# Performance work log

Measured on AMD Instinct MI355X. Metric: run time of the kernel, lower is better.

## Reference

```python
import jax, jax.numpy as jnp
import numpy as np

D_MODEL = 1024
NUM_HEADS = 16
SEQ_LEN = 2048
WINDOW_SIZES = (5, 10, 20, 40)


def _avg_gaussian_mask(seq_len, dtype=jnp.float32):
    # mask[i,j] = exp(-(i-j)^2/(2 w^2)) if j <= i else 0; averaged over 4 windows.
    i = jnp.arange(seq_len, dtype=dtype)[:, None]
    j = jnp.arange(seq_len, dtype=dtype)[None, :]
    d2 = (i - j) ** 2
    lower = (j <= i)
    masks = [jnp.where(lower, jnp.exp(-d2 / (2.0 * w * w)), 0.0) for w in WINDOW_SIZES]
    return sum(masks) / len(WINDOW_SIZES)  # [S, S]


def setup_inputs() -> dict:
    key = jax.random.key(0)
    ks = jax.random.split(key, 11)
    B, S, D = 2, SEQ_LEN, D_MODEL
    std = 1.0 / np.sqrt(D)
    inp = {
        "Q": jax.random.normal(ks[0], (B, S, D), jnp.float32),
        "K": jax.random.normal(ks[1], (B, S, D), jnp.float32),
        "V": jax.random.normal(ks[2], (B, S, D), jnp.float32),
        "Wq": jax.random.uniform(ks[3], (D, D), jnp.float32, -std, std),
        "bq": jax.random.uniform(ks[4], (D,), jnp.float32, -std, std),
        "Wk": jax.random.uniform(ks[5], (D, D), jnp.float32, -std, std),
        "bk": jax.random.uniform(ks[6], (D,), jnp.float32, -std, std),
        "Wv": jax.random.uniform(ks[7], (D, D), jnp.float32, -std, std),
        "bv": jax.random.uniform(ks[8], (D,), jnp.float32, -std, std),
        "Wo": jax.random.uniform(ks[9], (D, D), jnp.float32, -std, std),
        "bo": jax.random.uniform(ks[10], (D,), jnp.float32, -std, std),
    }
    return inp


def reference(Q, K, V, Wq, bq, Wk, bk, Wv, bv, Wo, bo):
    B, S, D = Q.shape
    H, dk = NUM_HEADS, D // NUM_HEADS

    def proj(x, W, b):
        # torch Linear: x @ W^T + b, then split heads -> [B, H, S, dk]
        y = x @ W.T + b
        return y.reshape(B, S, H, dk).transpose(0, 2, 1, 3)

    q = proj(Q, Wq, bq)
    k = proj(K, Wk, bk)
    v = proj(V, Wv, bv)

    # mean over mask dim of (scores + mask_m) == scores + mean(mask)
    avg_mask = _avg_gaussian_mask(S, q.dtype)  # [S, S]
    scores = jnp.einsum('bhqd,bhkd->bhqk', q, k) / jnp.sqrt(jnp.asarray(dk, q.dtype))
    scores = scores + avg_mask  # broadcast over [B, H]
    probs = jax.nn.softmax(scores, axis=-1)
    out = jnp.einsum('bhqk,bhkd->bhqd', probs, v)
    out = out.transpose(0, 2, 1, 3).reshape(B, S, D)
    return out @ Wo.T + bo
```

## Files before the change

kernel.cpp:

```cpp
#include <hip/hip_runtime.h>
#include <hip/hip_bf16.h>


#define S_LEN 2048
#define D_MODEL 1024
#define NHEADS 16
#define DK 64
#define BATCH 2
#define M_ROWS (BATCH * S_LEN)
#define LOG2E 1.4426950408889634f

typedef float f32x4 __attribute__((ext_vector_type(4)));
typedef short s16x8 __attribute__((ext_vector_type(8)));
typedef unsigned short u16x4 __attribute__((ext_vector_type(4)));
typedef unsigned u32x2 __attribute__((ext_vector_type(2)));

__device__ __forceinline__ unsigned short f2bf(float f) {
    unsigned u = __builtin_bit_cast(unsigned, f);
    u = (u + 0x7FFFu + ((u >> 16) & 1u)) >> 16;
    return (unsigned short)u;
}

__device__ __forceinline__ float fast_exp2(float x) {
    float r;
    asm("v_exp_f32 %0, %1" : "=v"(r) : "v"(x));
    return r;
}

__device__ __forceinline__ unsigned cvt_pk_bf16(float a, float b) {
    unsigned r;
    asm("v_cvt_pk_bf16_f32 %0, %1, %2" : "=v"(r) : "v"(a), "v"(b));
    return r;
}

__device__ __forceinline__ float max3f(float a, float b, float c) {
    float r;
    asm("v_max3_f32 %0, %1, %2, %3" : "=v"(r) : "v"(a), "v"(b), "v"(c));
    return r;
}

#define GLD16(gptr, lptr)                                                     \
    __builtin_amdgcn_global_load_lds(                                         \
        (const __attribute__((address_space(1))) void*)(gptr),                \
        (__attribute__((address_space(3))) void*)(lptr), 16, 0, 0)

__global__ void mask_kernel(float* __restrict__ mtab) {
    int d = blockIdx.x * 256 + threadIdx.x;
    if (d < S_LEN) {
        float d2 = (float)d * (float)d;
        mtab[d] = LOG2E * 0.25f * (__expf(-d2 * (1.0f / 50.0f)) +
                                   __expf(-d2 * (1.0f / 200.0f)) +
                                   __expf(-d2 * (1.0f / 800.0f)) +
                                   __expf(-d2 * (1.0f / 3200.0f)));
    }
}

__global__ __launch_bounds__(256) void convert_kernel(
    const float* __restrict__ Q, const float* __restrict__ K,
    const float* __restrict__ V,
    const float* __restrict__ Wq, const float* __restrict__ Wk,
    const float* __restrict__ Wv, const float* __restrict__ Wo,
    unsigned short* __restrict__ Qb, unsigned short* __restrict__ Kb,
    unsigned short* __restrict__ Vb,
    unsigned short* __restrict__ Wqb, unsigned short* __restrict__ Wkb,
    unsigned short* __restrict__ Wvb, unsigned short* __restrict__ Wob)
{
    const int XN = M_ROWS * D_MODEL / 8;
    const int WN = D_MODEL * D_MODEL / 8;
    int i = blockIdx.x * 256 + threadIdx.x;
    const float* src;
    unsigned short* dst;
    int off;
    if (i < 3 * XN) {
        if (i < XN)          { src = Q; dst = Qb; off = i; }
        else if (i < 2 * XN) { src = K; dst = Kb; off = i - XN; }
        else                 { src = V; dst = Vb; off = i - 2 * XN; }
    } else {
        int j = i - 3 * XN;
        if (j < WN)          { src = Wq; dst = Wqb; off = j; }
        else if (j < 2 * WN) { src = Wk; dst = Wkb; off = j - WN; }
        else if (j < 3 * WN) { src = Wv; dst = Wvb; off = j - 2 * WN; }
        else                 { src = Wo; dst = Wob; off = j - 3 * WN; }
    }
    f32x4 v0 = *(const f32x4*)(src + (size_t)off * 8);
    f32x4 v1 = *(const f32x4*)(src + (size_t)off * 8 + 4);
    s16x8 o;
#pragma unroll
    for (int j = 0; j < 4; ++j) {
        o[j]     = (short)f2bf(v0[j]);
        o[j + 4] = (short)f2bf(v1[j]);
    }
    *(s16x8*)(dst + (size_t)off * 8) = o;
}

__device__ __forceinline__ void gemm_core_128(
    const unsigned short* __restrict__ A, const unsigned short* __restrict__ B,
    unsigned short* As, unsigned short* Bs,
    int m0, int n0, int K, int tid, f32x4 acc[4][4])
{
    const int wid  = tid >> 6;
    const int lane = tid & 63;
    const int g    = lane >> 4;
    const int c    = lane & 15;
    const int wm   = wid >> 1;
    const int wn   = wid & 1;

    const int srow   = tid >> 3;
    const int schunk = tid & 7;

    for (int kt = 0; kt < K / 64; ++kt) {
        const int k0 = kt * 64;
        __syncthreads();
#pragma unroll
        for (int r = 0; r < 4; ++r) {
            const int row = r * 32 + srow;
            GLD16(A + (size_t)(m0 + row) * K + k0 + schunk * 8,
                  &As[(r * 256 + wid * 64) * 8]);
        }
#pragma unroll
        for (int r = 0; r < 4; ++r) {
            const int row = r * 32 + srow;
            GLD16(B + (size_t)(n0 + row) * K + k0 + schunk * 8,
                  &Bs[(r * 256 + wid * 64) * 8]);
        }
        __syncthreads();

        s16x8 a[2][4];
#pragma unroll
        for (int ks = 0; ks < 2; ++ks)
#pragma unroll
            for (int mf = 0; mf < 4; ++mf)
                a[ks][mf] = *(const s16x8*)
                    &As[(wm * 64 + mf * 16 + c) * 64 + ks * 32 + g * 8];
#pragma unroll
        for (int ks = 0; ks < 2; ++ks) {
#pragma unroll
            for (int nf = 0; nf < 4; ++nf) {
                s16x8 b = *(const s16x8*)
                    &Bs[(wn * 64 + nf * 16 + c) * 64 + ks * 32 + g * 8];
#pragma unroll
                for (int mf = 0; mf < 4; ++mf)
                    acc[mf][nf] = __builtin_amdgcn_mfma_f32_16x16x32_bf16(
                        a[ks][mf], b, acc[mf][nf], 0, 0, 0);
            }
        }
    }
}

__global__ __launch_bounds__(256) void proj_gemm(
    const unsigned short* __restrict__ Qx, const unsigned short* __restrict__ Kx,
    const unsigned short* __restrict__ Vx,
    const unsigned short* __restrict__ Wq, const unsigned short* __restrict__ Wk,
    const unsigned short* __restrict__ Wv,
    const float* __restrict__ bq, const float* __restrict__ bk,
    const float* __restrict__ bv,
    unsigned short* __restrict__ qo, unsigned short* __restrict__ ko,
    unsigned short* __restrict__ vo)
{
    const int z = blockIdx.z;
    const unsigned short* X = (z == 0) ? Qx : (z == 1) ? Kx : Vx;
    const unsigned short* W = (z == 0) ? Wq : (z == 1) ? Wk : Wv;
    const float* bias       = (z == 0) ? bq : (z == 1) ? bk : bv;
    unsigned short* out     = (z == 0) ? qo : (z == 1) ? ko : vo;
    const float scale = (z == 0) ? (0.125f * LOG2E) : 1.0f;

    __shared__ unsigned short As[128 * 64];
    __shared__ unsigned short Bs[128 * 64];

    const int tid = threadIdx.x;
    const int m0  = blockIdx.x * 128;
    const int n0  = blockIdx.y * 128;

    f32x4 acc[4][4];
#pragma unroll
    for (int i = 0; i < 4; ++i)
#pragma unroll
        for (int j = 0; j < 4; ++j) acc[i][j] = (f32x4){0.f, 0.f, 0.f, 0.f};

    gemm_core_128(X, W, As, Bs, m0, n0, D_MODEL, tid, acc);

    const int lane = tid & 63;
    const int g    = lane >> 4;
    const int c    = lane & 15;
    const int wm   = (tid >> 6) >> 1;
    const int wn   = (tid >> 6) & 1;

#pragma unroll
    for (int mf = 0; mf < 4; ++mf) {
#pragma unroll
        for (int nf = 0; nf < 4; ++nf) {
            const int o = n0 + wn * 64 + nf * 16 + c;
            const float bv_ = bias[o];
            const int h  = o >> 6;
            const int dd = o & 63;
#pragma unroll
            for (int r = 0; r < 4; ++r) {
                const int m = m0 + wm * 64 + mf * 16 + g * 4 + r;
                const int b = m >> 11;
                const int s = m & (S_LEN - 1);
                const float val = (acc[mf][nf][r] + bv_) * scale;
                out[(((size_t)(b * NHEADS + h)) * S_LEN + s) * DK + dd] = f2bf(val);
            }
        }
    }
}

__global__ __launch_bounds__(256) void out_gemm(
    const unsigned short* __restrict__ A,
    const unsigned short* __restrict__ W,
    const float* __restrict__ bias,
    float* __restrict__ out)
{
    __shared__ unsigned short As[128 * 64];
    __shared__ unsigned short Bs[128 * 64];

    const int tid = threadIdx.x;
    const int m0  = blockIdx.x * 128;
    const int n0  = blockIdx.y * 128;

    f32x4 acc[4][4];
#pragma unroll
    for (int i = 0; i < 4; ++i)
#pragma unroll
        for (int j = 0; j < 4; ++j) acc[i][j] = (f32x4){0.f, 0.f, 0.f, 0.f};

    gemm_core_128(A, W, As, Bs, m0, n0, D_MODEL, tid, acc);

    const int lane = tid & 63;
    const int g    = lane >> 4;
    const int c    = lane & 15;
    const int wm   = (tid >> 6) >> 1;
    const int wn   = (tid >> 6) & 1;

#pragma unroll
    for (int mf = 0; mf < 4; ++mf) {
#pragma unroll
        for (int nf = 0; nf < 4; ++nf) {
            const int o = n0 + wn * 64 + nf * 16 + c;
            const float bv_ = bias[o];
#pragma unroll
            for (int r = 0; r < 4; ++r) {
                const int m = m0 + wm * 64 + mf * 16 + g * 4 + r;
                out[(size_t)m * D_MODEL + o] = acc[mf][nf][r] + bv_;
            }
        }
    }
}

#define VSWZ(row) ((((row) >> 1) & 7) << 4)

__global__ __launch_bounds__(512) void attn_kernel(
    const unsigned short* __restrict__ qh,
    const unsigned short* __restrict__ kh,
    const unsigned short* __restrict__ vh,
    const float* __restrict__ mask_tab,
    unsigned short* __restrict__ attn_out)
{
    __shared__ float mtab[S_LEN];
    __shared__ unsigned short Kt[64 * 64];
    __shared__ unsigned short Vt[64 * 64];
    __shared__ unsigned short Pt[8][16 * 64];

    const int tid  = threadIdx.x;
    const int wid  = tid >> 6;
    const int lane = tid & 63;
    const int g    = lane >> 4;
    const int c    = lane & 15;
    const int bh   = blockIdx.y;
    const int b    = bh >> 4;
    const int h    = bh & 15;
    const int q0w  = blockIdx.x * 128 + wid * 16;

    *(f32x4*)&mtab[tid * 4] = *(const f32x4*)&mask_tab[tid * 4];

    const size_t head_off = (size_t)bh * S_LEN * DK;
    const unsigned short* qp = qh + head_off;
    const unsigned short* kp = kh + head_off;
    const unsigned short* vp = vh + head_off;

    s16x8 aq[2];
    {
        const unsigned short* qrow = qp + (size_t)(q0w + c) * DK;
        aq[0] = *(const s16x8*)(qrow + g * 8);
        aq[1] = *(const s16x8*)(qrow + 32 + g * 8);
    }

    f32x4 acc_o[4];
#pragma unroll
    for (int nf = 0; nf < 4; ++nf) acc_o[nf] = (f32x4){0.f, 0.f, 0.f, 0.f};
    float m_l = -1e30f, l_l = 0.f;

    const int srowK = tid >> 3;
    const int soffE = (tid & 7) * 8;
    const int vd0   = (tid & 31) * 2;
    const int vkq   = (tid >> 5) * 4;

    s16x8 kreg;
    unsigned vreg[4];
    kreg = *(const s16x8*)&kp[(size_t)srowK * DK + soffE];
#pragma unroll
    for (int i = 0; i < 4; ++i)
        vreg[i] = *(const unsigned*)&vp[(size_t)(vkq + i) * DK + vd0];

    unsigned short* Ptw = Pt[wid];

    for (int kt = 0; kt < S_LEN / 64; ++kt) {
        const int k0 = kt * 64;
        __syncthreads();

        *(s16x8*)((char*)Kt + srowK * 128 + ((soffE * 2) ^ ((srowK & 7) << 4))) = kreg;
        {
            u16x4 lo4, hi4;
#pragma unroll
            for (int i = 0; i < 4; ++i) {
                lo4[i] = (unsigned short)vreg[i];
                hi4[i] = (unsigned short)(vreg[i] >> 16);
            }
            *(u16x4*)((char*)Vt + vd0 * 128 + ((vkq * 2) ^ VSWZ(vd0))) = lo4;
            *(u16x4*)((char*)Vt + (vd0 + 1) * 128 +
                      ((vkq * 2) ^ VSWZ(vd0 + 1))) = hi4;
        }
        if (kt < S_LEN / 64 - 1) {
            const int k1 = k0 + 64;
            kreg = *(const s16x8*)&kp[(size_t)(k1 + srowK) * DK + soffE];
#pragma unroll
            for (int i = 0; i < 4; ++i)
                vreg[i] = *(const unsigned*)&vp[(size_t)(k1 + vkq + i) * DK + vd0];
        }
        __syncthreads();

        f32x4 st[4];
        __builtin_amdgcn_s_setprio(1);
#pragma unroll
        for (int nf = 0; nf < 4; ++nf) {
            st[nf] = (f32x4){0.f, 0.f, 0.f, 0.f};
#pragma unroll
            for (int f = 0; f < 2; ++f) {
                const int row = nf * 16 + c;
                s16x8 kf = *(const s16x8*)((const char*)Kt + row * 128 +
                                           ((f * 64 + g * 16) ^ ((row & 7) << 4)));
                st[nf] = __builtin_amdgcn_mfma_f32_16x16x32_bf16(
                    kf, aq[f], st[nf], 0, 0, 0);
            }
        }
        __builtin_amdgcn_s_setprio(0);

        const int diff = q0w - k0;
        if (diff >= -15 && diff <= 510) {
            const int dbase = q0w + c - k0;
#pragma unroll
            for (int nf = 0; nf < 4; ++nf) {
#pragma unroll
                for (int r = 0; r < 4; ++r) {
                    const int d = dbase - (nf * 16 + g * 4 + r);
                    if (d >= 0) st[nf][r] += mtab[d];
                }
            }
        }

        float tm = st[0][0];
        tm = max3f(tm, st[0][1], st[0][2]);
        tm = max3f(tm, st[0][3], st[1][0]);
        tm = max3f(tm, st[1][1], st[1][2]);
        tm = max3f(tm, st[1][3], st[2][0]);
        tm = max3f(tm, st[2][1], st[2][2]);
        tm = max3f(tm, st[2][3], st[3][0]);
        tm = max3f(tm, st[3][1], st[3][2]);
        tm = fmaxf(tm, st[3][3]);
        tm = fmaxf(tm, __shfl_xor(tm, 16));
        tm = fmaxf(tm, __shfl_xor(tm, 32));

        if (__any(tm > m_l + 8.0f)) {
            const float mnew = fmaxf(m_l, tm);
            const float csc  = fast_exp2(m_l - mnew);
            m_l = mnew;
            l_l *= csc;
            f32x4 cscv;
#pragma unroll
            for (int r = 0; r < 4; ++r) cscv[r] = __shfl(csc, g * 4 + r);
#pragma unroll
            for (int nf = 0; nf < 4; ++nf) acc_o[nf] *= cscv;
        }

#pragma unroll
        for (int nf = 0; nf < 4; ++nf)
#pragma unroll
            for (int r = 0; r < 4; ++r)
                st[nf][r] = fast_exp2(st[nf][r] - m_l);
        {
            f32x4 s4 = (st[0] + st[1]) + (st[2] + st[3]);
            float ps = (s4[0] + s4[1]) + (s4[2] + s4[3]);
            ps += __shfl_xor(ps, 16);
            ps += __shfl_xor(ps, 32);
            l_l += ps;
        }

#pragma unroll
        for (int nf = 0; nf < 4; ++nf) {
            u32x2 pk;
            pk[0] = cvt_pk_bf16(st[nf][0], st[nf][1]);
            pk[1] = cvt_pk_bf16(st[nf][2], st[nf][3]);
            *(u32x2*)((char*)Ptw + c * 128 +
                      ((nf * 32 + g * 8) ^ ((c & 7) << 4))) = pk;
        }

        __builtin_amdgcn_s_setprio(1);
#pragma unroll
        for (int f = 0; f < 2; ++f) {
            s16x8 pa = *(const s16x8*)((const char*)Ptw + c * 128 +
                                       ((f * 64 + g * 16) ^ ((c & 7) << 4)));
#pragma unroll
            for (int nf = 0; nf < 4; ++nf) {
                const int row = nf * 16 + c;
                s16x8 vb = *(const s16x8*)((const char*)Vt + row * 128 +
                                           ((f * 64 + g * 16) ^ VSWZ(row)));
                acc_o[nf] = __builtin_amdgcn_mfma_f32_16x16x32_bf16(
                    pa, vb, acc_o[nf], 0, 0, 0);
            }
        }
        __builtin_amdgcn_s_setprio(0);
    }

    float lq[4];
#pragma unroll
    for (int r = 0; r < 4; ++r) lq[r] = __shfl(l_l, g * 4 + r);
#pragma unroll
    for (int nf = 0; nf < 4; ++nf) {
#pragma unroll
        for (int r = 0; r < 4; ++r) {
            const int i_glob = q0w + g * 4 + r;
            const int d = nf * 16 + c;
            const float o = acc_o[nf][r] / lq[r];
            attn_out[((size_t)(b * S_LEN + i_glob)) * D_MODEL + h * DK + d] = f2bf(o);
        }
    }
}

extern "C" void kernel_launch(void* const* d_in, const int* in_sizes, int n_in,
                              void* d_out, int out_size, void* d_ws, size_t ws_size,
                              hipStream_t stream) {
    const float* Q  = (const float*)d_in[0];
    const float* K  = (const float*)d_in[1];
    const float* V  = (const float*)d_in[2];
    const float* Wq = (const float*)d_in[3];
    const float* bq = (const float*)d_in[4];
    const float* Wk = (const float*)d_in[5];
    const float* bk = (const float*)d_in[6];
    const float* Wv = (const float*)d_in[7];
    const float* bv = (const float*)d_in[8];
    const float* Wo = (const float*)d_in[9];
    const float* bo = (const float*)d_in[10];
    float* out = (float*)d_out;

    const size_t XE = (size_t)M_ROWS * D_MODEL;
    const size_t WE = (size_t)D_MODEL * D_MODEL;
    unsigned short* qh  = (unsigned short*)d_ws;
    unsigned short* kh  = qh + XE;
    unsigned short* vh  = kh + XE;
    unsigned short* ah  = vh + XE;
    unsigned short* Qb  = ah + XE;
    unsigned short* Kb  = Qb + XE;
    unsigned short* Vb  = Kb + XE;
    unsigned short* Wqb = Vb + XE;
    unsigned short* Wkb = Wqb + WE;
    unsigned short* Wvb = Wkb + WE;
    unsigned short* Wob = Wvb + WE;
    float* mtab = (float*)(Wob + WE);

    mask_kernel<<<dim3(S_LEN / 256), 256, 0, stream>>>(mtab);
    convert_kernel<<<dim3((3 * XE / 8 + 4 * WE / 8) / 256), 256, 0, stream>>>(
        Q, K, V, Wq, Wk, Wv, Wo, Qb, Kb, Vb, Wqb, Wkb, Wvb, Wob);
    proj_gemm<<<dim3(M_ROWS / 128, D_MODEL / 128, 3), 256, 0, stream>>>(
        Qb, Kb, Vb, Wqb, Wkb, Wvb, bq, bk, bv, qh, kh, vh);
    attn_kernel<<<dim3(S_LEN / 128, BATCH * NHEADS), 512, 0, stream>>>(
        qh, kh, vh, mtab, ah);
    out_gemm<<<dim3(M_ROWS / 128, D_MODEL / 128), 256, 0, stream>>>(
        ah, Wob, bo, out);
}
```

Measured before the change: 153.0 us.

## Fuse mask into convert, swizzle block order, defer softmax row-sum reductions

```diff
diff --git a/kernel.cpp b/kernel.cpp
--- a/kernel.cpp
+++ b/kernel.cpp
@@ -43,17 +43,6 @@
     __builtin_amdgcn_global_load_lds(                                         \
         (const __attribute__((address_space(1))) void*)(gptr),                \
         (__attribute__((address_space(3))) void*)(lptr), 16, 0, 0)
-
-__global__ void mask_kernel(float* __restrict__ mtab) {
-    int d = blockIdx.x * 256 + threadIdx.x;
-    if (d < S_LEN) {
-        float d2 = (float)d * (float)d;
-        mtab[d] = LOG2E * 0.25f * (__expf(-d2 * (1.0f / 50.0f)) +
-                                   __expf(-d2 * (1.0f / 200.0f)) +
-                                   __expf(-d2 * (1.0f / 800.0f)) +
-                                   __expf(-d2 * (1.0f / 3200.0f)));
-    }
-}
 
 __global__ __launch_bounds__(256) void convert_kernel(
     const float* __restrict__ Q, const float* __restrict__ K,
@@ -63,11 +52,24 @@
     unsigned short* __restrict__ Qb, unsigned short* __restrict__ Kb,
     unsigned short* __restrict__ Vb,
     unsigned short* __restrict__ Wqb, unsigned short* __restrict__ Wkb,
-    unsigned short* __restrict__ Wvb, unsigned short* __restrict__ Wob)
+    unsigned short* __restrict__ Wvb, unsigned short* __restrict__ Wob,
+    float* __restrict__ mtab)
 {
     const int XN = M_ROWS * D_MODEL / 8;
     const int WN = D_MODEL * D_MODEL / 8;
+    const int TOT = 3 * XN + 4 * WN;
     int i = blockIdx.x * 256 + threadIdx.x;
+    if (i >= TOT) {
+        int d = i - TOT;
+        if (d < S_LEN) {
+            float d2 = (float)d * (float)d;
+            mtab[d] = LOG2E * 0.25f * (__expf(-d2 * (1.0f / 50.0f)) +
+                                       __expf(-d2 * (1.0f / 200.0f)) +
+                                       __expf(-d2 * (1.0f / 800.0f)) +
+                                       __expf(-d2 * (1.0f / 3200.0f)));
+        }
+        return;
+    }
     const float* src;
     unsigned short* dst;
     int off;
@@ -168,8 +170,10 @@
     __shared__ unsigned short Bs[128 * 64];
 
     const int tid = threadIdx.x;
-    const int m0  = blockIdx.x * 128;
-    const int n0  = blockIdx.y * 128;
+    const int flat = blockIdx.y * 32 + blockIdx.x;
+    const int sw   = (flat & 7) * 32 + (flat >> 3);
+    const int m0   = (sw & 31) * 128;
+    const int n0   = (sw >> 5) * 128;
 
     f32x4 acc[4][4];
 #pragma unroll
@@ -215,8 +219,10 @@
     __shared__ unsigned short Bs[128 * 64];
 
     const int tid = threadIdx.x;
-    const int m0  = blockIdx.x * 128;
-    const int n0  = blockIdx.y * 128;
+    const int flat = blockIdx.y * 32 + blockIdx.x;
+    const int sw   = (flat & 7) * 32 + (flat >> 3);
+    const int m0   = (sw & 31) * 128;
+    const int n0   = (sw >> 5) * 128;
 
     f32x4 acc[4][4];
 #pragma unroll
@@ -266,10 +272,14 @@
     const int lane = tid & 63;
     const int g    = lane >> 4;
     const int c    = lane & 15;
-    const int bh   = blockIdx.y;
+
+    const int flat = blockIdx.y * 16 + blockIdx.x;
+    const int sw   = (flat & 7) * 64 + (flat >> 3);
+    const int bh   = sw >> 4;
+    const int bx   = sw & 15;
     const int b    = bh >> 4;
     const int h    = bh & 15;
-    const int q0w  = blockIdx.x * 128 + wid * 16;
+    const int q0w  = bx * 128 + wid * 16;
 
     *(f32x4*)&mtab[tid * 4] = *(const f32x4*)&mask_tab[tid * 4];
 
@@ -288,7 +298,8 @@
     f32x4 acc_o[4];
 #pragma unroll
     for (int nf = 0; nf < 4; ++nf) acc_o[nf] = (f32x4){0.f, 0.f, 0.f, 0.f};
-    float m_l = -1e30f, l_l = 0.f;
+    float m_l = -1e30f;
+    f32x4 lsum = (f32x4){0.f, 0.f, 0.f, 0.f};
 
     const int srowK = tid >> 3;
     const int soffE = (tid & 7) * 8;
@@ -358,8 +369,7 @@
             }
         }
 
-        float tm = st[0][0];
-        tm = max3f(tm, st[0][1], st[0][2]);
+        float tm = max3f(st[0][0], st[0][1], st[0][2]);
         tm = max3f(tm, st[0][3], st[1][0]);
         tm = max3f(tm, st[1][1], st[1][2]);
         tm = max3f(tm, st[1][3], st[2][0]);
@@ -367,14 +377,14 @@
         tm = max3f(tm, st[2][3], st[3][0]);
         tm = max3f(tm, st[3][1], st[3][2]);
         tm = fmaxf(tm, st[3][3]);
-        tm = fmaxf(tm, __shfl_xor(tm, 16));
-        tm = fmaxf(tm, __shfl_xor(tm, 32));
 
         if (__any(tm > m_l + 8.0f)) {
+            tm = fmaxf(tm, __shfl_xor(tm, 16));
+            tm = fmaxf(tm, __shfl_xor(tm, 32));
             const float mnew = fmaxf(m_l, tm);
             const float csc  = fast_exp2(m_l - mnew);
             m_l = mnew;
-            l_l *= csc;
+            lsum *= csc;
             f32x4 cscv;
 #pragma unroll
             for (int r = 0; r < 4; ++r) cscv[r] = __shfl(csc, g * 4 + r);
@@ -387,13 +397,7 @@
 #pragma unroll
             for (int r = 0; r < 4; ++r)
                 st[nf][r] = fast_exp2(st[nf][r] - m_l);
-        {
-            f32x4 s4 = (st[0] + st[1]) + (st[2] + st[3]);
-            float ps = (s4[0] + s4[1]) + (s4[2] + s4[3]);
-            ps += __shfl_xor(ps, 16);
-            ps += __shfl_xor(ps, 32);
-            l_l += ps;
-        }
+        lsum += (st[0] + st[1]) + (st[2] + st[3]);
 
 #pragma unroll
         for (int nf = 0; nf < 4; ++nf) {
@@ -421,17 +425,20 @@
         __builtin_amdgcn_s_setprio(0);
     }
 
-    float lq[4];
-#pragma unroll
-    for (int r = 0; r < 4; ++r) lq[r] = __shfl(l_l, g * 4 + r);
+    float l = (lsum[0] + lsum[1]) + (lsum[2] + lsum[3]);
+    l += __shfl_xor(l, 16);
+    l += __shfl_xor(l, 32);
+    f32x4 linv;
+#pragma unroll
+    for (int r = 0; r < 4; ++r) linv[r] = 1.0f / __shfl(l, g * 4 + r);
 #pragma unroll
     for (int nf = 0; nf < 4; ++nf) {
 #pragma unroll
         for (int r = 0; r < 4; ++r) {
             const int i_glob = q0w + g * 4 + r;
             const int d = nf * 16 + c;
-            const float o = acc_o[nf][r] / lq[r];
-            attn_out[((size_t)(b * S_LEN + i_glob)) * D_MODEL + h * DK + d] = f2bf(o);
+            attn_out[((size_t)(b * S_LEN + i_glob)) * D_MODEL + h * DK + d] =
+                f2bf(acc_o[nf][r] * linv[r]);
         }
     }
 }
@@ -467,13 +474,12 @@
     unsigned short* Wob = Wvb + WE;
     float* mtab = (float*)(Wob + WE);
 
-    mask_kernel<<<dim3(S_LEN / 256), 256, 0, stream>>>(mtab);
-    convert_kernel<<<dim3((3 * XE / 8 + 4 * WE / 8) / 256), 256, 0, stream>>>(
-        Q, K, V, Wq, Wk, Wv, Wo, Qb, Kb, Vb, Wqb, Wkb, Wvb, Wob);
-    proj_gemm<<<dim3(M_ROWS / 128, D_MODEL / 128, 3), 256, 0, stream>>>(
+    convert_kernel<<<dim3((3 * XE / 8 + 4 * WE / 8) / 256 + 8), 256, 0, stream>>>(
+        Q, K, V, Wq, Wk, Wv, Wo, Qb, Kb, Vb, Wqb, Wkb, Wvb, Wob, mtab);
+    proj_gemm<<<dim3(32, 8, 3), 256, 0, stream>>>(
         Qb, Kb, Vb, Wqb, Wkb, Wvb, bq, bk, bv, qh, kh, vh);
-    attn_kernel<<<dim3(S_LEN / 128, BATCH * NHEADS), 512, 0, stream>>>(
+    attn_kernel<<<dim3(16, 32), 512, 0, stream>>>(
         qh, kh, vh, mtab, ah);
-    out_gemm<<<dim3(M_ROWS / 128, D_MODEL / 128), 256, 0, stream>>>(
+    out_gemm<<<dim3(32, 8), 256, 0, stream>>>(
         ah, Wob, bo, out);
 }
```

Result: faster. 135.4 us (-11.5%).
